# Kernel tuning notes

Measured on AMD Instinct MI355X. Metric: run time of the kernel, lower is better.

The kernel has to match this reference:

```python
import jax, jax.numpy as jnp
import numpy as np
from jax import lax

RF = 19       # receptive field: layers*(kernel-1)+1 = 3*6+1
WINDOW = 12
N_MIX = 2
K = 20        # subgraph_size (top-k per row)
GDEP = 2
ALPHA = 0.05  # propalpha
EPS = 1e-5


def conv2d(x, w, b):
    # x: [N,C,H,W], w: [O,I,1,k], valid conv along time (last) axis
    o = lax.conv_general_dilated(x, w, (1, 1), 'VALID',
                                 dimension_numbers=('NCHW', 'OIHW', 'NCHW'))
    return o + b[None, :, None, None]


def dilated_inception(x, ws, b):
    # ws: kernels [co, ci, k] for k in (2,3,6,7); dilation factor is 1 here
    outs = [lax.conv_general_dilated(x, w[:, :, None, :], (1, 1), 'VALID',
                                     dimension_numbers=('NCHW', 'OIHW', 'NCHW'))
            for w in ws]
    L = outs[-1].shape[-1]  # truncate to shortest (largest kernel) length
    out = jnp.concatenate([o[..., -L:] for o in outs], axis=1)
    return out + b[None, :, None, None]


def build_adj(e1, e2, l1w, l1b, l2w, l2b):
    # e1,e2: [M2,N,D] embedding tables (idx = arange -> full table)
    # torch Linear: y = x @ W.T + b, W: [out,in]
    nv1 = jnp.einsum('mnd,mod->mno', e1, l1w) + l1b[:, None, :]
    nv2 = jnp.einsum('mnd,mod->mno', e2, l2w) + l2b[:, None, :]
    a = jnp.einsum('mnd,mkd->mnk', nv1, nv2)  # [M2, N, N] per-block adjacency
    rows = [jnp.concatenate([a[i * N_MIX + j] for j in range(N_MIX)], axis=1)
            for i in range(N_MIX)]
    adj = jnp.concatenate(rows, axis=0)  # [NT, NT]
    _, t = lax.top_k(adj, K)  # per-row top-k indices
    mask = jnp.zeros_like(adj).at[jnp.arange(adj.shape[0])[:, None], t].set(1.0)
    return adj * mask


def mixprop(x, adj, w, b):
    a = adj + jnp.eye(adj.shape[0], dtype=adj.dtype)
    a = a / jnp.sum(a, axis=1, keepdims=True)  # row-normalize
    h = x
    outs = [h]
    for _ in range(GDEP):
        h = ALPHA * x + (1.0 - ALPHA) * jnp.einsum('ncwl,vw->ncvl', h, a)
        outs.append(h)
    ho = jnp.concatenate(outs, axis=1)  # [B,(GDEP+1)*C,V,L]
    return jnp.einsum('ncvl,oc->novl', ho, w) + b[None, :, None, None]


def layernorm(x, w, b):
    # torch F.layer_norm over all dims except batch; idx = arange -> full affine
    mu = jnp.mean(x, axis=(1, 2, 3), keepdims=True)
    var = jnp.mean((x - mu) ** 2, axis=(1, 2, 3), keepdims=True)
    return (x - mu) * lax.rsqrt(var + EPS) * w[None] + b[None]


def setup_inputs() -> dict:
    keys = iter(jax.random.split(jax.random.key(0), 80))
    def rn(shape, s=0.1):
        return s * jax.random.normal(next(keys), shape, dtype=jnp.float32)
    d = {}
    d['x_in'] = jax.random.normal(next(keys), (32, 12, 500, 4), dtype=jnp.float32)
    d['start_w'] = rn((32, 1, 1, 1)); d['start_b'] = rn((32,))
    d['skip0_w'] = rn((64, 1, 1, 19)); d['skip0_b'] = rn((64,))
    d['emb1'] = rn((3, 4, 500, 40)); d['emb2'] = rn((3, 4, 500, 40))
    d['lin1_w'] = rn((3, 4, 40, 40)); d['lin1_b'] = rn((3, 4, 40))
    d['lin2_w'] = rn((3, 4, 40, 40)); d['lin2_b'] = rn((3, 4, 40))
    d['g1_w'] = rn((3, 32, 96)); d['g1_b'] = rn((3, 32))
    d['g2_w'] = rn((3, 32, 96)); d['g2_b'] = rn((3, 32))
    for pref in ('filt', 'gate'):
        for k in (2, 3, 6, 7):
            d[f'{pref}_w{k}'] = rn((3, 8, 32, k))
        d[f'{pref}_b'] = rn((3, 32))
    for i, L in zip((1, 2, 3), (13, 7, 1)):
        d[f'skip_w{i}'] = rn((64, 32, 1, L)); d[f'skip_b{i}'] = rn((64,))
        d[f'norm_w{i}'] = jnp.ones((32, 1000, L), jnp.float32)
        d[f'norm_b{i}'] = jnp.zeros((32, 1000, L), jnp.float32)
    d['skipE_w'] = rn((64, 32, 1, 1)); d['skipE_b'] = rn((64,))
    d['end1_w'] = rn((128, 64, 1, 1)); d['end1_b'] = rn((128,))
    d['end2_w'] = rn((12, 128, 1, 1)); d['end2_b'] = rn((12,))
    return d


def reference(x_in, start_w, start_b, skip0_w, skip0_b, emb1, emb2,
              lin1_w, lin1_b, lin2_w, lin2_b, g1_w, g1_b, g2_w, g2_b,
              filt_w2, filt_w3, filt_w6, filt_w7, filt_b,
              gate_w2, gate_w3, gate_w6, gate_w7, gate_b,
              skip_w1, skip_b1, skip_w2, skip_b2, skip_w3, skip_b3,
              norm_w1, norm_b1, norm_w2, norm_b2, norm_w3, norm_b3,
              skipE_w, skipE_b, end1_w, end1_b, end2_w, end2_b):
    feat = x_in[..., :-2]  # drop last 2 'time' features
    # split per-mode feature and stack along node dim: [B,T,2N,1]
    inp = jnp.concatenate([feat[..., 0:1], feat[..., 1:2]], axis=2)
    inp = jnp.transpose(inp, (0, 3, 2, 1))  # [B,1,2N,T]
    inp = jnp.pad(inp, ((0, 0), (0, 0), (0, 0), (RF - WINDOW, 0)))
    x = conv2d(inp, start_w, start_b)       # [B,32,1000,19]
    skip = conv2d(inp, skip0_w, skip0_b)    # [B,64,1000,1] (dropout=eval no-op)
    filt_ws = (filt_w2, filt_w3, filt_w6, filt_w7)
    gate_ws = (gate_w2, gate_w3, gate_w6, gate_w7)
    skips = ((skip_w1, skip_b1), (skip_w2, skip_b2), (skip_w3, skip_b3))
    norms = ((norm_w1, norm_b1), (norm_w2, norm_b2), (norm_w3, norm_b3))
    for i in range(3):
        adp = build_adj(emb1[i], emb2[i], lin1_w[i], lin1_b[i], lin2_w[i], lin2_b[i])
        residual = x
        x = mixprop(x, adp, g1_w[i], g1_b[i]) + mixprop(x, adp.T, g2_w[i], g2_b[i])
        f = jnp.tanh(dilated_inception(x, [w[i] for w in filt_ws], filt_b[i]))
        g = jax.nn.sigmoid(dilated_inception(x, [w[i] for w in gate_ws], gate_b[i]))
        x = f * g
        sw, sb = skips[i]
        skip = conv2d(x, sw, sb) + skip
        x = x + residual[..., -x.shape[3]:]
        nw, nb = norms[i]
        x = layernorm(x, nw, nb)
    skip = conv2d(x, skipE_w, skipE_b) + skip
    x = jax.nn.relu(skip)
    x = jax.nn.relu(conv2d(x, end1_w, end1_b))
    return conv2d(x, end2_w, end2_b)  # [B, horizon*out_dim0=12, 1000, 1]
```

## Files before the change

### kernel.cpp

```cpp
#include <hip/hip_runtime.h>
#include <math.h>


#define ALPHA_C 0.05f
#define EPS_C 1e-5f
#define NBC 32
#define CSCT_CAP 140000

__device__ float g_inp[32 * 19 * 1000];
__device__ float g_skip[32 * 64 * 1000];
__device__ __align__(16) float g_nv1[240000];
__device__ __align__(16) float g_nv2[240000];
__device__ __align__(16) int   g_tkcol[60000];
__device__ __align__(16) float g_tkval[60000];
__device__ float g_inv1[3000];
__device__ int   g_colcnt[3000];
__device__ float g_colsum[3000];
__device__ int   g_rp2[3 * 1001 + 1];
__device__ int   g_fill[3000];
__device__ int   g_cscr[60000];
__device__ float g_cscv[60000];
__device__ float g_inv2[3000];
__device__ float g_stats[3 * 64];
__device__ __align__(16) int2 g_pk1T[60000];
__device__ __align__(16) int2 g_cscT[3 * CSCT_CAP];
__device__ int   g_perm[3 * 1024];
__device__ int   g_degT[3 * 1024];
__device__ int   g_iperm[3 * 1000];
__device__ int   g_tOff[3 * 17];
__device__ float g_B0[(size_t)NBC * 32 * 19 * 1000];
__device__ float g_B1[(size_t)NBC * 32 * 19 * 1000];
__device__ float g_B2[(size_t)NBC * 32 * 19 * 1000];
__device__ float g_B3[(size_t)NBC * 32 * 19 * 1000];
__device__ float g_B4[(size_t)NBC * 32 * 19 * 1000];
__device__ float g_B5[(size_t)NBC * 32 * 19 * 1000];

__device__ __forceinline__ float* bufsel(int s)
{
    switch (s) {
        case 0: return g_B0;
        case 1: return g_B1;
        case 2: return g_B2;
        case 3: return g_B3;
        case 4: return g_B4;
        default: return g_B5;
    }
}

__global__ void k_init()
{
    int i = blockIdx.x * 256 + threadIdx.x;
    if (i < 3000) { g_colcnt[i] = 0; g_colsum[i] = 0.f; g_fill[i] = 0; }
    if (i < 192) g_stats[i] = 0.f;
}

__global__ void k_out_zero(float* __restrict__ out, int n)
{
    int i = blockIdx.x * 256 + threadIdx.x;
    if (i < n) out[i] = 0.0f;
}

__global__ void k_marker(float* __restrict__ out, float v)
{
    if (threadIdx.x == 0) out[0] = v;
}


__global__ void k_build_inp(const float* __restrict__ xin)
{
    int i = blockIdx.x * 256 + threadIdx.x;
    if (i >= 32 * 19 * 1000) return;
    int v = i % 1000;
    int t = (i / 1000) % 19;
    int b = i / 19000;
    float val = 0.f;
    if (t >= 7) {
        int tt = t - 7;
        int n = (v < 500) ? v : v - 500;
        int f = (v < 500) ? 0 : 1;
        val = xin[((b * 12 + tt) * 500 + n) * 4 + f];
    }
    g_inp[i] = val;
}

__global__ void k_nv(const float* __restrict__ e1, const float* __restrict__ e2,
                     const float* __restrict__ w1, const float* __restrict__ b1,
                     const float* __restrict__ w2, const float* __restrict__ b2)
{
    int i = blockIdx.x * 256 + threadIdx.x;
    if (i >= 12 * 500 * 40) return;
    int o = i % 40;
    int n = (i / 40) % 500;
    int m = i / (40 * 500);
    const float4* p1 = (const float4*)(e1 + (m * 500 + n) * 40);
    const float4* pw1 = (const float4*)(w1 + (m * 40 + o) * 40);
    const float4* p2 = (const float4*)(e2 + (m * 500 + n) * 40);
    const float4* pw2 = (const float4*)(w2 + (m * 40 + o) * 40);
    float a1 = b1[m * 40 + o], a2 = b2[m * 40 + o];
    for (int d = 0; d < 10; ++d) {
        float4 x1 = p1[d], y1 = pw1[d];
        float4 x2 = p2[d], y2 = pw2[d];
        a1 += x1.x * y1.x; a1 += x1.y * y1.y; a1 += x1.z * y1.z; a1 += x1.w * y1.w;
        a2 += x2.x * y2.x; a2 += x2.y * y2.y; a2 += x2.z * y2.z; a2 += x2.w * y2.w;
    }
    g_nv1[i] = a1;
    g_nv2[i] = a2;
}

__global__ __launch_bounds__(256) void k_adj_topk()
{
    __shared__ float row[1000];
    __shared__ float wvv[4];
    __shared__ int wvi[4];
    __shared__ int selc[20];
    __shared__ float selv[20];
    int li = blockIdx.x / 1000;
    int r = blockIdx.x % 1000;
    int tid = threadIdx.x;
    int wv = tid >> 6, lane = tid & 63;
    int bi = r / 500, n = r % 500;
    for (int c = tid; c < 1000; c += 256) {
        int bj = c / 500, k = c % 500;
        int mg = li * 4 + 2 * bi + bj;
        const float4* a = (const float4*)(g_nv1 + (mg * 500 + n) * 40);
        const float4* b = (const float4*)(g_nv2 + (mg * 500 + k) * 40);
        float acc = 0.f;
#pragma unroll
        for (int d = 0; d < 10; ++d) {
            float4 av = a[d], bv = b[d];
            acc += av.x * bv.x; acc += av.y * bv.y;
            acc += av.z * bv.z; acc += av.w * bv.w;
        }
        row[c] = acc;
    }
    __syncthreads();
    for (int sel = 0; sel < 20; ++sel) {
        float bv = -INFINITY;
        int bidx = 0;
        for (int c = tid; c < 1000; c += 256) {
            float x = row[c];
            if (x > bv) { bv = x; bidx = c; }
        }
#pragma unroll
        for (int m = 1; m < 64; m <<= 1) {
            float ov = __shfl_xor(bv, m);
            int oi = __shfl_xor(bidx, m);
            if (ov > bv || (ov == bv && oi < bidx)) { bv = ov; bidx = oi; }
        }
        if (lane == 0) { wvv[wv] = bv; wvi[wv] = bidx; }
        __syncthreads();
        if (tid == 0) {
            float fv = wvv[0];
            int fi = wvi[0];
#pragma unroll
            for (int k = 1; k < 4; ++k) {
                float ov = wvv[k];
                int oi = wvi[k];
                if (ov > fv || (ov == fv && oi < fi)) { fv = ov; fi = oi; }
            }
            int ci = fi;
            if (ci < 0 || ci > 999) ci = sel;
            selc[sel] = ci;
            selv[sel] = fv;
            g_tkcol[(li * 1000 + r) * 20 + sel] = ci;
            g_tkval[(li * 1000 + r) * 20 + sel] = fv;
            row[ci] = -INFINITY;
        }
        __syncthreads();
    }
    if (tid < 20) {
        atomicAdd(&g_colcnt[li * 1000 + selc[tid]], 1);
        atomicAdd(&g_colsum[li * 1000 + selc[tid]], selv[tid]);
    }
    if (tid == 0) {
        float s = 0.f;
        for (int j = 0; j < 20; ++j) s += selv[j];
        g_inv1[li * 1000 + r] = 1.f / (s + 1.f);
    }
}

__global__ __launch_bounds__(256) void k_scan()
{
    __shared__ int s[1000];
    int li = blockIdx.x;
    int tid = threadIdx.x;
    for (int i = tid; i < 1000; i += 256) s[i] = g_colcnt[li * 1000 + i];
    __syncthreads();
    if (tid == 0) {
        int run = 0;
        for (int i = 0; i < 1000; ++i) { int c = s[i]; s[i] = run; run += c; }
        g_rp2[li * 1001 + 1000] = run;
    }
    __syncthreads();
    for (int i = tid; i < 1000; i += 256) {
        g_rp2[li * 1001 + i] = s[i];
        g_inv2[li * 1000 + i] = 1.f / (g_colsum[li * 1000 + i] + 1.f);
    }
}

__global__ __launch_bounds__(256) void k_permsort()
{
    __shared__ int deg[1000];
    __shared__ int tmax[16];
    int li = blockIdx.x;
    int tid = threadIdx.x;
    for (int v = tid; v < 1000; v += 256)
        deg[v] = g_rp2[li * 1001 + v + 1] - g_rp2[li * 1001 + v];
    __syncthreads();
    for (int v = tid; v < 1000; v += 256) {
        int d = deg[v];
        int r = 0;
        for (int u = 0; u < 1000; ++u) {
            int du = deg[u];
            r += (du > d) || (du == d && u < v);
        }
        g_perm[li * 1024 + r] = v;
        g_degT[li * 1024 + r] = d;
        g_iperm[li * 1000 + v] = r;
        if ((r & 63) == 0) tmax[r >> 6] = d;
    }
    if (tid < 24) {
        g_perm[li * 1024 + 1000 + tid] = -1;
        g_degT[li * 1024 + 1000 + tid] = 0;
    }
    __syncthreads();
    if (tid == 0) {
        int off = 0;
        for (int t = 0; t < 16; ++t) {
            g_tOff[li * 17 + t] = off;
            off += 64 * tmax[t];
        }
        g_tOff[li * 17 + 16] = off;
    }
}

__global__ void k_scatter()
{
    int i = blockIdx.x * 256 + threadIdx.x;
    if (i >= 3 * 20000) return;
    int li = i / 20000;
    int e = i % 20000;
    int r = e / 20;
    int c = g_tkcol[i];
    if (c < 0) c = 0;
    if (c > 999) c = 999;
    float v = g_tkval[i];
    int pos = g_rp2[li * 1001 + c] + atomicAdd(&g_fill[li * 1000 + c], 1);
    if (pos < 0) pos = 0;
    if (pos > 19999) pos = 19999;
    g_cscr[li * 20000 + pos] = r;
    g_cscv[li * 20000 + pos] = v;
}

__global__ void k_packT1()
{
    int i = blockIdx.x * 256 + threadIdx.x;
    if (i >= 60000) return;
    int li = i / 20000;
    int e = i % 20000;
    int v = e / 20, j = e % 20;
    int c1 = g_tkcol[i];
    if (c1 < 0) c1 = 0;
    if (c1 > 999) c1 = 999;
    g_pk1T[li * 20000 + j * 1000 + v] = make_int2(c1 * 16, __float_as_int(g_tkval[i]));
}

__global__ void k_packT2()
{
    int i = blockIdx.x * 256 + threadIdx.x;
    if (i >= 3000) return;
    int li = i / 1000, v = i % 1000;
    int r = g_iperm[li * 1000 + v];
    int t = r >> 6, ln = r & 63;
    int j0 = g_rp2[li * 1001 + v];
    int d = g_rp2[li * 1001 + v + 1] - j0;
    int base = g_tOff[li * 17 + t];
    for (int j = 0; j < d; ++j) {
        int row = g_cscr[li * 20000 + j0 + j];
        if (row < 0) row = 0;
        if (row > 999) row = 999;
        int pos = base + j * 64 + ln;
        if (pos >= 0 && pos < CSCT_CAP)
            g_cscT[li * CSCT_CAP + pos] =
                make_int2(row * 16, __float_as_int(g_cscv[li * 20000 + j0 + j]));
    }
}


__global__ __launch_bounds__(256) void k_skip0(const float* __restrict__ w,
                                               const float* __restrict__ bb)
{
    __shared__ float s_inp[19 * 32];
    __shared__ float s_w[64 * 19];
    int b = blockIdx.y;
    int v0 = blockIdx.x * 32;
    int tid = threadIdx.x;
    for (int i = tid; i < 64 * 19; i += 256) s_w[i] = w[i];
    for (int i = tid; i < 19 * 32; i += 256) {
        int t = i / 32, vl = i % 32;
        int v = v0 + vl;
        s_inp[i] = (v < 1000) ? g_inp[(b * 19 + t) * 1000 + v] : 0.f;
    }
    __syncthreads();
    for (int e = tid; e < 64 * 32; e += 256) {
        int o = e / 32, vl = e % 32;
        int v = v0 + vl;
        if (v >= 1000) continue;
        float acc = bb[o];
#pragma unroll
        for (int t = 0; t < 19; ++t) acc += s_w[o * 19 + t] * s_inp[t * 32 + vl];
        g_skip[(b * 64 + o) * 1000 + v] = acc;
    }
}

__global__ __launch_bounds__(256, 5) void k_prop4(int xsel, int o1s, int o2s, int o3s, int o4s,
                                                  int li, int CH, int li0,
                                                  const float* __restrict__ sw,
                                                  const float* __restrict__ sb)
{
    __shared__ float4 S[2000];
    const float* X = bufsel(xsel);
    float* o1 = bufsel(o1s);
    float* o2 = bufsel(o2s);
    float* o3 = bufsel(o3s);
    float* o4 = bufsel(o4s);
    const int2* pkT = g_pk1T + li * 20000;
    const int2* cT = g_cscT + (size_t)li * CSCT_CAP;
    const int* prm = g_perm + li * 1024;
    const int* dgT = g_degT + li * 1024;
    const int* tOf = g_tOff + li * 17;
    const float* iv1 = g_inv1 + li * 1000;
    const float* iv2 = g_inv2 + li * 1000;
    int n = blockIdx.y;
    int ch0 = blockIdx.x * 4;
    size_t gb = ((size_t)n * CH + ch0) * 1000;
    int tid = threadIdx.x;
    int wv = tid >> 6, lane = tid & 63;
    char* Ub = (char*)S;
    char* Wb = (char*)(S + 1000);
    float4* U4 = S;
    float4* W4 = S + 1000;

    auto csr_hop = [&](const char* sbuf, float4* dst) {
        for (int it = 0; it < 4; ++it) {
            int v = it * 256 + tid;
            if (v >= 1000) break;
            const int2* mp = pkT + v;
            float4 a = *(const float4*)(sbuf + (size_t)v * 16);
#pragma unroll
            for (int jb = 0; jb < 5; ++jb) {
                int2 e0 = mp[(jb * 4 + 0) * 1000];
                int2 e1 = mp[(jb * 4 + 1) * 1000];
                int2 e2 = mp[(jb * 4 + 2) * 1000];
                int2 e3 = mp[(jb * 4 + 3) * 1000];
                float w0 = __int_as_float(e0.y), w1 = __int_as_float(e1.y);
                float w2 = __int_as_float(e2.y), w3 = __int_as_float(e3.y);
                float4 x0 = *(const float4*)(sbuf + e0.x);
                float4 x1 = *(const float4*)(sbuf + e1.x);
                float4 x2 = *(const float4*)(sbuf + e2.x);
                float4 x3 = *(const float4*)(sbuf + e3.x);
                a.x += w0 * x0.x + w1 * x1.x + w2 * x2.x + w3 * x3.x;
                a.y += w0 * x0.y + w1 * x1.y + w2 * x2.y + w3 * x3.y;
                a.z += w0 * x0.z + w1 * x1.z + w2 * x2.z + w3 * x3.z;
                a.w += w0 * x0.w + w1 * x1.w + w2 * x2.w + w3 * x3.w;
            }
            float s = iv1[v];
            a.x *= s; a.y *= s; a.z *= s; a.w *= s;
            dst[v] = a;
        }
    };

    auto csc_hop = [&](const char* sbuf, float4* dst) {
        for (int o = 0; o < 4; ++o) {
            int tile = o * 4 + ((o & 1) ? (3 - wv) : wv);
            int r = tile * 64 + lane;
            int v = prm[r];
            if (v < 0) continue;
            int d = dgT[r];
            const int2* mp = cT + tOf[tile] + lane;
            float4 a = *(const float4*)(sbuf + (size_t)v * 16);
            int j = 0;
            for (; j + 4 <= d; j += 4) {
                int2 e0 = mp[(j + 0) * 64];
                int2 e1 = mp[(j + 1) * 64];
                int2 e2 = mp[(j + 2) * 64];
                int2 e3 = mp[(j + 3) * 64];
                float w0 = __int_as_float(e0.y), w1 = __int_as_float(e1.y);
                float w2 = __int_as_float(e2.y), w3 = __int_as_float(e3.y);
                float4 x0 = *(const float4*)(sbuf + e0.x);
                float4 x1 = *(const float4*)(sbuf + e1.x);
                float4 x2 = *(const float4*)(sbuf + e2.x);
                float4 x3 = *(const float4*)(sbuf + e3.x);
                a.x += w0 * x0.x + w1 * x1.x + w2 * x2.x + w3 * x3.x;
                a.y += w0 * x0.y + w1 * x1.y + w2 * x2.y + w3 * x3.y;
                a.z += w0 * x0.z + w1 * x1.z + w2 * x2.z + w3 * x3.z;
                a.w += w0 * x0.w + w1 * x1.w + w2 * x2.w + w3 * x3.w;
            }
            for (; j < d; ++j) {
                int2 e = mp[j * 64];
                float w = __int_as_float(e.y);
                float4 x = *(const float4*)(sbuf + e.x);
                a.x += w * x.x; a.y += w * x.y; a.z += w * x.z; a.w += w * x.w;
            }
            float s = iv2[v];
            a.x *= s; a.y *= s; a.z *= s; a.w *= s;
            dst[v] = a;
        }
    };

    auto stage_x = [&](float4* dst) {
        if (li0) {
            float swv0 = sw[(ch0 + 0) / 19], sbv0 = sb[(ch0 + 0) / 19];
            float swv1 = sw[(ch0 + 1) / 19], sbv1 = sb[(ch0 + 1) / 19];
            float swv2 = sw[(ch0 + 2) / 19], sbv2 = sb[(ch0 + 2) / 19];
            float swv3 = sw[(ch0 + 3) / 19], sbv3 = sb[(ch0 + 3) / 19];
            const float* i0 = g_inp + (n * 19 + (ch0 + 0) % 19) * 1000;
            const float* i1 = g_inp + (n * 19 + (ch0 + 1) % 19) * 1000;
            const float* i2 = g_inp + (n * 19 + (ch0 + 2) % 19) * 1000;
            const float* i3 = g_inp + (n * 19 + (ch0 + 3) % 19) * 1000;
            for (int it = 0; it < 4; ++it) {
                int v = it * 256 + tid;
                if (v >= 1000) break;
                float4 t;
                t.x = swv0 * i0[v] + sbv0;
                t.y = swv1 * i1[v] + sbv1;
                t.z = swv2 * i2[v] + sbv2;
                t.w = swv3 * i3[v] + sbv3;
                dst[v] = t;
            }
        } else {
            for (int it = 0; it < 4; ++it) {
                int v = it * 256 + tid;
                if (v >= 1000) break;
                float4 t;
                t.x = X[gb + v];
                t.y = X[gb + 1000 + v];
                t.z = X[gb + 2000 + v];
                t.w = X[gb + 3000 + v];
                dst[v] = t;
            }
        }
    };

    stage_x(U4);
    __syncthreads();

    csr_hop(Ub, W4);
    __syncthreads();

    for (int it = 0; it < 4; ++it) {
        int v = it * 256 + tid;
        if (v >= 1000) break;
        float4 t = W4[v];
        o1[gb + v] = t.x;
        o1[gb + 1000 + v] = t.y;
        o1[gb + 2000 + v] = t.z;
        o1[gb + 3000 + v] = t.w;
    }
    csr_hop(Wb, U4);
    __syncthreads();

    for (int it = 0; it < 4; ++it) {
        int v = it * 256 + tid;
        if (v >= 1000) break;
        float4 t = U4[v];
        o2[gb + v] = t.x;
        o2[gb + 1000 + v] = t.y;
        o2[gb + 2000 + v] = t.z;
        o2[gb + 3000 + v] = t.w;
    }
    stage_x(W4);
    __syncthreads();

    csc_hop(Wb, U4);
    __syncthreads();

    for (int it = 0; it < 4; ++it) {
        int v = it * 256 + tid;
        if (v >= 1000) break;
        float4 t = U4[v];
        o3[gb + v] = t.x;
        o3[gb + 1000 + v] = t.y;
        o3[gb + 2000 + v] = t.z;
        o3[gb + 3000 + v] = t.w;
    }
    csc_hop(Ub, W4);
    __syncthreads();

    for (int it = 0; it < 4; ++it) {
        int v = it * 256 + tid;
        if (v >= 1000) break;
        float4 t = W4[v];
        o4[gb + v] = t.x;
        o4[gb + 1000 + v] = t.y;
        o4[gb + 2000 + v] = t.z;
        o4[gb + 3000 + v] = t.w;
    }
}

__global__ __launch_bounds__(256) void k_mix(int xs, int h1s, int h2s, int h3s, int h4s, int ms,
                                             const float* __restrict__ g1w, const float* __restrict__ g2w,
                                             const float* __restrict__ g1b, const float* __restrict__ g2b,
                                             int P, int li0,
                                             const float* __restrict__ sw_,
                                             const float* __restrict__ sb_)
{
    __shared__ float sW[5 * 1024];
    __shared__ float sB[32];
    __shared__ float sWS[32];
    __shared__ float sSB[32];
    int tid = threadIdx.x;
    const float A = ALPHA_C, Bq = 1.f - ALPHA_C;
    for (int i = tid; i < 1024; i += 256) {
        int o = i >> 5, c = i & 31;
        float w1 = g1w[o * 96 + 32 + c], w2 = g1w[o * 96 + 64 + c];
        float w3 = g2w[o * 96 + 32 + c], w4 = g2w[o * 96 + 64 + c];
        sW[i]        = g1w[o * 96 + c] + g2w[o * 96 + c] + A * (w1 + w2 + w3 + w4);
        sW[1024 + i] = Bq * (w1 + A * w2);
        sW[2048 + i] = Bq * Bq * w2;
        sW[3072 + i] = Bq * (w3 + A * w4);
        sW[4096 + i] = Bq * Bq * w4;
    }
    if (tid < 32) sB[tid] = g1b[tid] + g2b[tid];
    __syncthreads();
    if (li0 && tid < 32) {
        float as = 0.f, ab = 0.f;
        for (int c = 0; c < 32; ++c) {
            float w = sW[tid * 32 + c];
            as += w * sw_[c];
            ab += w * sb_[c];
        }
        sWS[tid] = as;
        sSB[tid] = ab;
    }
    if (li0) __syncthreads();
    int n = blockIdx.y;
    int p = blockIdx.x * 256 + tid;
    if (p >= P) return;
    const float* srcs[5] = {bufsel(xs), bufsel(h1s), bufsel(h2s), bufsel(h3s), bufsel(h4s)};
    float acc[32];
    int st0;
    if (li0) {
        float xv = g_inp[(size_t)n * 19000 + p];
#pragma unroll
        for (int o = 0; o < 32; ++o) acc[o] = sB[o] + sSB[o] + sWS[o] * xv;
        st0 = 1;
    } else {
#pragma unroll
        for (int o = 0; o < 32; ++o) acc[o] = sB[o];
        st0 = 0;
    }
    for (int st = st0; st < 5; ++st) {
        const float* src = srcs[st] + (size_t)n * 32 * P + p;
        const float* w = &sW[st * 1024];
        for (int c = 0; c < 32; ++c) {
            float hv = src[(size_t)c * P];
#pragma unroll
            for (int o = 0; o < 32; ++o) acc[o] += w[o * 32 + c] * hv;
        }
    }
    float* XM = bufsel(ms) + (size_t)n * 32 * P + p;
#pragma unroll
    for (int o = 0; o < 32; ++o) XM[(size_t)o * P] = acc[o];
}

template <int LIN>
__global__ __launch_bounds__(256) void k_incept(int xmsel, int xgsel,
                                                const float* __restrict__ fw2, const float* __restrict__ fw3,
                                                const float* __restrict__ fw6, const float* __restrict__ fw7,
                                                const float* __restrict__ fb,
                                                const float* __restrict__ gw2, const float* __restrict__ gw3,
                                                const float* __restrict__ gw6, const float* __restrict__ gw7,
                                                const float* __restrict__ gb,
                                                const float* __restrict__ skw, const float* __restrict__ skb)
{
    const int LOUT = LIN - 6;
    const float* XM = bufsel(xmsel);
    float* XG = bufsel(xgsel);
    __shared__ float sx[32 * 8 * LIN];
    __shared__ float sxg[32 * 8 * LOUT];
    int tid = threadIdx.x;
    int n = blockIdx.y, v0 = blockIdx.x * 8;
    for (int i = tid; i < 32 * LIN * 8; i += 256) {
        int vl = i & 7;
        int l = (i >> 3) % LIN;
        int c = i / (8 * LIN);
        sx[(c * 8 + vl) * LIN + l] = XM[(((size_t)n * 32 + c) * LIN + l) * 1000 + v0 + vl];
    }
    __syncthreads();
    int co = tid >> 3, vl = tid & 7;
    int s = co >> 3, co_s = co & 7;
    const int ksz[4] = {2, 3, 6, 7};
    int k = ksz[s];
    const float* fw = (s == 0) ? fw2 : ((s == 1) ? fw3 : ((s == 2) ? fw6 : fw7));
    const float* gw = (s == 0) ? gw2 : ((s == 1) ? gw3 : ((s == 2) ? gw6 : gw7));
    float accf[LOUT], accg[LOUT];
    float bf = fb[co], bg = gb[co];
#pragma unroll
    for (int l = 0; l < LOUT; ++l) { accf[l] = bf; accg[l] = bg; }
    for (int c = 0; c < 32; ++c) {
        const float* xp = &sx[(c * 8 + vl) * LIN];
        for (int j = 0; j < k; ++j) {
            float wf = fw[(co_s * 32 + c) * k + j];
            float wg = gw[(co_s * 32 + c) * k + j];
            int base = 7 - k + j;
#pragma unroll
            for (int l = 0; l < LOUT; ++l) {
                float xv = xp[base + l];
                accf[l] += wf * xv;
                accg[l] += wg * xv;
            }
        }
    }
    size_t ob = ((size_t)n * 32 + co) * LOUT * 1000 + v0 + vl;
#pragma unroll
    for (int l = 0; l < LOUT; ++l) {
        float g = tanhf(accf[l]) * (1.f / (1.f + expf(-accg[l])));
        XG[ob + (size_t)l * 1000] = g;
        sxg[(co * 8 + vl) * LOUT + l] = g;
    }
    __syncthreads();
    int obk = tid >> 3;
    for (int half = 0; half < 2; ++half) {
        int o = obk + 32 * half;
        float acc = skb[o];
        for (int c = 0; c < 32; ++c) {
            const float* wp = &skw[((size_t)o * 32 + c) * LOUT];
            const float* xp = &sxg[(c * 8 + vl) * LOUT];
#pragma unroll
            for (int l = 0; l < LOUT; ++l) acc += wp[l] * xp[l];
        }
        size_t si = ((size_t)n * 64 + o) * 1000 + v0 + vl;
        g_skip[si] += acc;
    }
}

__global__ __launch_bounds__(256) void k_resid_stats(int xnsel, int xpsel,
                                                     int li, int LIN, int LOUT, int li0,
                                                     const float* __restrict__ sw_,
                                                     const float* __restrict__ sb_)
{
    float* XN = bufsel(xnsel);
    const float* Xp = bufsel(xpsel);
    float* stats = g_stats + li * 64;
    int n = blockIdx.y;
    int S = 32 * LOUT * 1000;
    int tid = threadIdx.x;
    int gsz = gridDim.x * 256;
    float sum = 0.f, ss = 0.f;
    for (int idx = blockIdx.x * 256 + tid; idx < S; idx += gsz) {
        int v = idx % 1000;
        int l = (idx / 1000) % LOUT;
        int c = idx / (1000 * LOUT);
        float r;
        if (li0)
            r = sw_[c] * g_inp[(n * 19 + l + 6) * 1000 + v] + sb_[c];
        else
            r = Xp[(((size_t)n * 32 + c) * LIN + l + (LIN - LOUT)) * 1000 + v];
        float y = XN[(size_t)n * S + idx] + r;
        XN[(size_t)n * S + idx] = y;
        sum += y;
        ss += y * y;
    }
    __shared__ float s1[256], s2[256];
    s1[tid] = sum;
    s2[tid] = ss;
    __syncthreads();
    for (int s = 128; s > 0; s >>= 1) {
        if (tid < s) { s1[tid] += s1[tid + s]; s2[tid] += s2[tid + s]; }
        __syncthreads();
    }
    if (tid == 0) {
        atomicAdd(&stats[n * 2], s1[0]);
        atomicAdd(&stats[n * 2 + 1], s2[0]);
    }
}

__global__ void k_norm(int xnsel, const float* __restrict__ nw,
                       const float* __restrict__ nb, int li, int LOUT)
{
    float* XN = bufsel(xnsel);
    const float* stats = g_stats + li * 64;
    int S = 32 * LOUT * 1000;
    long long total = (long long)NBC * S;
    long long stride = (long long)gridDim.x * 256;
    for (long long i = (long long)blockIdx.x * 256 + threadIdx.x; i < total; i += stride) {
        int n = (int)(i / S);
        int rem = (int)(i % S);
        int v = rem % 1000;
        int l = (rem / 1000) % LOUT;
        int c = rem / (1000 * LOUT);
        int widx = (c * 1000 + v) * LOUT + l;
        float cnt = (float)S;
        float mu = stats[n * 2] / cnt;
        float var = stats[n * 2 + 1] / cnt - mu * mu;
        float rs = rsqrtf(var + EPS_C);
        XN[i] = (XN[i] - mu) * rs * nw[widx] + nb[widx];
    }
}

__global__ __launch_bounds__(256) void k_final(int xsel,
                                               const float* __restrict__ ew, const float* __restrict__ eb,
                                               const float* __restrict__ e1w, const float* __restrict__ e1b,
                                               const float* __restrict__ e2w, const float* __restrict__ e2b,
                                               float* __restrict__ out)
{
    const float* X = bufsel(xsel);
    __shared__ float sxf[32 * 16];
    __shared__ float sk[64 * 16];
    __shared__ float s1[64 * 16];
    __shared__ float s2[128 * 16];
    int b = blockIdx.y, v0 = blockIdx.x * 16;
    int tid = threadIdx.x;
    for (int i = tid; i < 512; i += 256) {
        int c = i / 16, vl = i & 15;
        int v = v0 + vl;
        sxf[i] = (v < 1000) ? X[((size_t)b * 32 + c) * 1000 + v] : 0.f;
    }
    for (int i = tid; i < 1024; i += 256) {
        int o = i / 16, vl = i & 15;
        int v = v0 + vl;
        sk[i] = (v < 1000) ? g_skip[((size_t)b * 64 + o) * 1000 + v] : 0.f;
    }
    __syncthreads();
    for (int i = tid; i < 1024; i += 256) {
        int o = i / 16, vl = i & 15;
        float acc = sk[i] + eb[o];
        for (int c = 0; c < 32; ++c) acc += ew[o * 32 + c] * sxf[c * 16 + vl];
        s1[i] = fmaxf(acc, 0.f);
    }
    __syncthreads();
    for (int i = tid; i < 2048; i += 256) {
        int o = i / 16, vl = i & 15;
        float acc = e1b[o];
        for (int c = 0; c < 64; ++c) acc += e1w[o * 64 + c] * s1[c * 16 + vl];
        s2[i] = fmaxf(acc, 0.f);
    }
    __syncthreads();
    if (tid < 192) {
        int o = tid / 16, vl = tid & 15;
        int v = v0 + vl;
        if (v < 1000) {
            float acc = e2b[o];
            for (int c = 0; c < 128; ++c) acc += e2w[o * 128 + c] * s2[c * 16 + vl];
            out[((size_t)b * 12 + o) * 1000 + v] = acc;
        }
    }
}


static const int SZ_SORT[43] = {240000,240000,128,8192,12,1536,96,1536,2304,4608,
                                5376,96,9216,96,9216,96,1536,2304,4608,5376,
                                480,19200,480,19200,416000,224000,32000,416000,224000,32000,
                                64,1216,64,2048,64,64,64,26624,14336,2048,32,32,768000};
static const int SZ_DICT[43] = {768000,32,32,1216,64,240000,240000,19200,480,19200,
                                480,9216,96,9216,96,1536,2304,4608,5376,96,
                                1536,2304,4608,5376,96,26624,64,416000,416000,14336,
                                64,224000,224000,2048,64,32000,32000,2048,64,8192,128,1536,12};
static const int SZ_SIG[43]  = {768000,32,32,1216,64,240000,240000,19200,480,19200,
                                480,9216,96,9216,96,1536,2304,4608,5376,96,
                                1536,2304,4608,5376,96,26624,64,14336,64,2048,
                                64,416000,416000,224000,224000,32000,32000,2048,64,8192,128,1536,12};

extern "C" void kernel_launch(void* const* d_in, const int* in_sizes, int n_in,
                              void* d_out, int out_size, void* d_ws, size_t ws_size,
                              hipStream_t stream)
{
    (void)d_ws; (void)ws_size;
    const float *x_in, *start_w, *start_b, *skip0_w, *skip0_b;
    const float *emb1, *emb2, *lin1_w, *lin1_b, *lin2_w, *lin2_b;
    const float *g1_w, *g1_b, *g2_w, *g2_b;
    const float *filt_w[4], *filt_b, *gate_w[4], *gate_b;
    const float *skw[3], *skb[3], *nww[3], *nbb[3];
    const float *skipE_w, *skipE_b, *end1_w, *end1_b, *end2_w, *end2_b;
    float* outp = (float*)d_out;
    auto P = [&](int i) { return (const float*)d_in[i]; };
    auto match = [&](const int* tab) {
        if (n_in < 43) return false;
        for (int i = 0; i < 43; ++i) if (in_sizes[i] != tab[i]) return false;
        return true;
    };

    int fam = -1;
    if (match(SZ_SORT)) fam = 0;
    else if (match(SZ_DICT)) fam = 1;
    else if (match(SZ_SIG)) fam = 2;

    if (fam == 0) {
        emb1 = P(0); emb2 = P(1); end1_b = P(2); end1_w = P(3); end2_b = P(4); end2_w = P(5);
        filt_b = P(6); filt_w[0] = P(7); filt_w[1] = P(8); filt_w[2] = P(9); filt_w[3] = P(10);
        g1_b = P(11); g1_w = P(12); g2_b = P(13); g2_w = P(14);
        gate_b = P(15); gate_w[0] = P(16); gate_w[1] = P(17); gate_w[2] = P(18); gate_w[3] = P(19);
        lin1_b = P(20); lin1_w = P(21); lin2_b = P(22); lin2_w = P(23);
        nbb[0] = P(24); nbb[1] = P(25); nbb[2] = P(26);
        nww[0] = P(27); nww[1] = P(28); nww[2] = P(29);
        skip0_b = P(30); skip0_w = P(31); skipE_b = P(32); skipE_w = P(33);
        skb[0] = P(34); skb[1] = P(35); skb[2] = P(36);
        skw[0] = P(37); skw[1] = P(38); skw[2] = P(39);
        start_b = P(40); start_w = P(41); x_in = P(42);
    } else if (fam == 1 || fam == 2) {
        x_in = P(0); start_w = P(1); start_b = P(2); skip0_w = P(3); skip0_b = P(4);
        emb1 = P(5); emb2 = P(6); lin1_w = P(7); lin1_b = P(8); lin2_w = P(9); lin2_b = P(10);
        g1_w = P(11); g1_b = P(12); g2_w = P(13); g2_b = P(14);
        filt_w[0] = P(15); filt_w[1] = P(16); filt_w[2] = P(17); filt_w[3] = P(18); filt_b = P(19);
        gate_w[0] = P(20); gate_w[1] = P(21); gate_w[2] = P(22); gate_w[3] = P(23); gate_b = P(24);
        if (fam == 1) {
            skw[0] = P(25); skb[0] = P(26); nww[0] = P(27); nbb[0] = P(28);
            skw[1] = P(29); skb[1] = P(30); nww[1] = P(31); nbb[1] = P(32);
            skw[2] = P(33); skb[2] = P(34); nww[2] = P(35); nbb[2] = P(36);
        } else {
            skw[0] = P(25); skb[0] = P(26); skw[1] = P(27); skb[1] = P(28);
            skw[2] = P(29); skb[2] = P(30);
            nww[0] = P(31); nbb[0] = P(32); nww[1] = P(33); nbb[1] = P(34);
            nww[2] = P(35); nbb[2] = P(36);
        }
        skipE_w = P(37); skipE_b = P(38); end1_w = P(39); end1_b = P(40);
        end2_w = P(41); end2_b = P(42);
    } else {
        k_out_zero<<<(out_size + 255) / 256, 256, 0, stream>>>(outp, out_size);
        k_marker<<<1, 64, 0, stream>>>(outp, 8192.0f);
        return;
    }

    k_init<<<12, 256, 0, stream>>>();
    k_build_inp<<<(32 * 19 * 1000 + 255) / 256, 256, 0, stream>>>(x_in);
    k_nv<<<(240000 + 255) / 256, 256, 0, stream>>>(emb1, emb2, lin1_w, lin1_b, lin2_w, lin2_b);
    k_adj_topk<<<3000, 256, 0, stream>>>();
    k_scan<<<3, 256, 0, stream>>>();
    k_permsort<<<3, 256, 0, stream>>>();
    k_scatter<<<(60000 + 255) / 256, 256, 0, stream>>>();
    k_packT1<<<(60000 + 255) / 256, 256, 0, stream>>>();
    k_packT2<<<12, 256, 0, stream>>>();

    k_skip0<<<dim3(32, NBC), 256, 0, stream>>>(skip0_w, skip0_b);

    int X = 0;
    int LIN = 19;
    for (int li = 0; li < 3; ++li) {
        int LOUT = LIN - 6;
        int Pp = 1000 * LIN;
        int li0 = (li == 0) ? 1 : 0;
        int hb[4], hn = 0;
        for (int b = 0; b < 6 && hn < 4; ++b)
            if (b != X && b != 1) hb[hn++] = b;
        int h1 = hb[0], h2 = hb[1], h3 = hb[2], h4 = hb[3];
        int CH = 32 * LIN;
        dim3 gg((unsigned)(CH / 4), NBC);

        k_prop4<<<gg, 256, 0, stream>>>(X, h1, h2, h3, h4, li, CH, li0, start_w, start_b);

        k_mix<<<dim3((Pp + 255) / 256, NBC), 256, 0, stream>>>(X, h1, h2, h3, h4, 1,
            g1_w + li * 3072, g2_w + li * 3072, g1_b + li * 32, g2_b + li * 32, Pp,
            li0, start_w, start_b);

        int XG = h1;
        if (LIN == 19)
            k_incept<19><<<dim3(125, NBC), 256, 0, stream>>>(1, XG,
                filt_w[0] + li * 512, filt_w[1] + li * 768, filt_w[2] + li * 1536, filt_w[3] + li * 1792,
                filt_b + li * 32,
                gate_w[0] + li * 512, gate_w[1] + li * 768, gate_w[2] + li * 1536, gate_w[3] + li * 1792,
                gate_b + li * 32, skw[li], skb[li]);
        else if (LIN == 13)
            k_incept<13><<<dim3(125, NBC), 256, 0, stream>>>(1, XG,
                filt_w[0] + li * 512, filt_w[1] + li * 768, filt_w[2] + li * 1536, filt_w[3] + li * 1792,
                filt_b + li * 32,
                gate_w[0] + li * 512, gate_w[1] + li * 768, gate_w[2] + li * 1536, gate_w[3] + li * 1792,
                gate_b + li * 32, skw[li], skb[li]);
        else
            k_incept<7><<<dim3(125, NBC), 256, 0, stream>>>(1, XG,
                filt_w[0] + li * 512, filt_w[1] + li * 768, filt_w[2] + li * 1536, filt_w[3] + li * 1792,
                filt_b + li * 32,
                gate_w[0] + li * 512, gate_w[1] + li * 768, gate_w[2] + li * 1536, gate_w[3] + li * 1792,
                gate_b + li * 32, skw[li], skb[li]);

        k_resid_stats<<<dim3(16, NBC), 256, 0, stream>>>(XG, X, li, LIN, LOUT,
                                                         li0, start_w, start_b);
        k_norm<<<2048, 256, 0, stream>>>(XG, nww[li], nbb[li], li, LOUT);

        X = XG;
        LIN = LOUT;
    }
    k_final<<<dim3(63, NBC), 256, 0, stream>>>(X, skipE_w, skipE_b,
                                               end1_w, end1_b, end2_w, end2_b, outp);
}
```

Baseline: 2.671 ms.

## Fuse residual add and norm stats into inception kernel; reuse staged input in prop

The residual add and the per-sample layernorm sum and sum-of-squares are folded into the inception epilogue, with a wave-shuffle reduction and atomics. This removes the separate k_resid_stats launch and its extra read and write of the activation tensor. In k_prop4 the staged input is kept in shared memory across the CSR and CSC hops, so it is no longer reloaded. The CSR hops also write their outputs to global memory directly instead of through a separate copy loop. The inception kernel takes on more per-thread work and extra global loads for the residual, and atomics now come from every block.

```diff
diff --git a/kernel.cpp b/kernel.cpp
--- a/kernel.cpp
+++ b/kernel.cpp
@@ -341,7 +341,7 @@
     float4* U4 = S;
     float4* W4 = S + 1000;
 
-    auto csr_hop = [&](const char* sbuf, float4* dst) {
+    auto csr_hop = [&](const char* sbuf, float4* dst, float* gout) {
         for (int it = 0; it < 4; ++it) {
             int v = it * 256 + tid;
             if (v >= 1000) break;
@@ -366,7 +366,11 @@
             }
             float s = iv1[v];
             a.x *= s; a.y *= s; a.z *= s; a.w *= s;
-            dst[v] = a;
+            if (dst) dst[v] = a;
+            gout[gb + v] = a.x;
+            gout[gb + 1000 + v] = a.y;
+            gout[gb + 2000 + v] = a.z;
+            gout[gb + 3000 + v] = a.w;
         }
     };
 
@@ -408,89 +412,64 @@
         }
     };
 
-    auto stage_x = [&](float4* dst) {
-        if (li0) {
-            float swv0 = sw[(ch0 + 0) / 19], sbv0 = sb[(ch0 + 0) / 19];
-            float swv1 = sw[(ch0 + 1) / 19], sbv1 = sb[(ch0 + 1) / 19];
-            float swv2 = sw[(ch0 + 2) / 19], sbv2 = sb[(ch0 + 2) / 19];
-            float swv3 = sw[(ch0 + 3) / 19], sbv3 = sb[(ch0 + 3) / 19];
-            const float* i0 = g_inp + (n * 19 + (ch0 + 0) % 19) * 1000;
-            const float* i1 = g_inp + (n * 19 + (ch0 + 1) % 19) * 1000;
-            const float* i2 = g_inp + (n * 19 + (ch0 + 2) % 19) * 1000;
-            const float* i3 = g_inp + (n * 19 + (ch0 + 3) % 19) * 1000;
-            for (int it = 0; it < 4; ++it) {
-                int v = it * 256 + tid;
-                if (v >= 1000) break;
-                float4 t;
-                t.x = swv0 * i0[v] + sbv0;
-                t.y = swv1 * i1[v] + sbv1;
-                t.z = swv2 * i2[v] + sbv2;
-                t.w = swv3 * i3[v] + sbv3;
-                dst[v] = t;
-            }
-        } else {
-            for (int it = 0; it < 4; ++it) {
-                int v = it * 256 + tid;
-                if (v >= 1000) break;
-                float4 t;
-                t.x = X[gb + v];
-                t.y = X[gb + 1000 + v];
-                t.z = X[gb + 2000 + v];
-                t.w = X[gb + 3000 + v];
-                dst[v] = t;
-            }
-        }
-    };
-
-    stage_x(U4);
-    __syncthreads();
-
-    csr_hop(Ub, W4);
+    if (li0) {
+        float swv0 = sw[(ch0 + 0) / 19], sbv0 = sb[(ch0 + 0) / 19];
+        float swv1 = sw[(ch0 + 1) / 19], sbv1 = sb[(ch0 + 1) / 19];
+        float swv2 = sw[(ch0 + 2) / 19], sbv2 = sb[(ch0 + 2) / 19];
+        float swv3 = sw[(ch0 + 3) / 19], sbv3 = sb[(ch0 + 3) / 19];
+        const float* i0 = g_inp + (n * 19 + (ch0 + 0) % 19) * 1000;
+        const float* i1 = g_inp + (n * 19 + (ch0 + 1) % 19) * 1000;
+        const float* i2 = g_inp + (n * 19 + (ch0 + 2) % 19) * 1000;
+        const float* i3 = g_inp + (n * 19 + (ch0 + 3) % 19) * 1000;
+        for (int it = 0; it < 4; ++it) {
+            int v = it * 256 + tid;
+            if (v >= 1000) break;
+            float4 t;
+            t.x = swv0 * i0[v] + sbv0;
+            t.y = swv1 * i1[v] + sbv1;
+            t.z = swv2 * i2[v] + sbv2;
+            t.w = swv3 * i3[v] + sbv3;
+            U4[v] = t;
+        }
+    } else {
+        for (int it = 0; it < 4; ++it) {
+            int v = it * 256 + tid;
+            if (v >= 1000) break;
+            float4 t;
+            t.x = X[gb + v];
+            t.y = X[gb + 1000 + v];
+            t.z = X[gb + 2000 + v];
+            t.w = X[gb + 3000 + v];
+            U4[v] = t;
+        }
+    }
+    __syncthreads();
+
+    csr_hop(Ub, W4, o1);
+    __syncthreads();
+
+    csr_hop(Wb, (float4*)nullptr, o2);
+    __syncthreads();
+
+    csc_hop(Ub, W4);
     __syncthreads();
 
     for (int it = 0; it < 4; ++it) {
         int v = it * 256 + tid;
         if (v >= 1000) break;
         float4 t = W4[v];
-        o1[gb + v] = t.x;
-        o1[gb + 1000 + v] = t.y;
-        o1[gb + 2000 + v] = t.z;
-        o1[gb + 3000 + v] = t.w;
-    }
-    csr_hop(Wb, U4);
+        o3[gb + v] = t.x;
+        o3[gb + 1000 + v] = t.y;
+        o3[gb + 2000 + v] = t.z;
+        o3[gb + 3000 + v] = t.w;
+    }
+    csc_hop(Wb, U4);
     __syncthreads();
 
     for (int it = 0; it < 4; ++it) {
         int v = it * 256 + tid;
         if (v >= 1000) break;
         float4 t = U4[v];
-        o2[gb + v] = t.x;
-        o2[gb + 1000 + v] = t.y;
-        o2[gb + 2000 + v] = t.z;
-        o2[gb + 3000 + v] = t.w;
-    }
-    stage_x(W4);
-    __syncthreads();
-
-    csc_hop(Wb, U4);
-    __syncthreads();
-
-    for (int it = 0; it < 4; ++it) {
-        int v = it * 256 + tid;
-        if (v >= 1000) break;
-        float4 t = U4[v];
-        o3[gb + v] = t.x;
-        o3[gb + 1000 + v] = t.y;
-        o3[gb + 2000 + v] = t.z;
-        o3[gb + 3000 + v] = t.w;
-    }
-    csc_hop(Ub, W4);
-    __syncthreads();
-
-    for (int it = 0; it < 4; ++it) {
-        int v = it * 256 + tid;
-        if (v >= 1000) break;
-        float4 t = W4[v];
         o4[gb + v] = t.x;
         o4[gb + 1000 + v] = t.y;
         o4[gb + 2000 + v] = t.z;
@@ -565,20 +544,26 @@
 }
 
 template <int LIN>
-__global__ __launch_bounds__(256) void k_incept(int xmsel, int xgsel,
+__global__ __launch_bounds__(256) void k_incept(int xmsel, int xgsel, int xpsel,
                                                 const float* __restrict__ fw2, const float* __restrict__ fw3,
                                                 const float* __restrict__ fw6, const float* __restrict__ fw7,
                                                 const float* __restrict__ fb,
                                                 const float* __restrict__ gw2, const float* __restrict__ gw3,
                                                 const float* __restrict__ gw6, const float* __restrict__ gw7,
                                                 const float* __restrict__ gb,
-                                                const float* __restrict__ skw, const float* __restrict__ skb)
+                                                const float* __restrict__ skw, const float* __restrict__ skb,
+                                                int li, int li0,
+                                                const float* __restrict__ sw_,
+                                                const float* __restrict__ sb_)
 {
     const int LOUT = LIN - 6;
     const float* XM = bufsel(xmsel);
     float* XG = bufsel(xgsel);
+    const float* Xp = bufsel(xpsel);
+    float* stats = g_stats + li * 64;
     __shared__ float sx[32 * 8 * LIN];
     __shared__ float sxg[32 * 8 * LOUT];
+    __shared__ float ws1[4], ws2[4];
     int tid = threadIdx.x;
     int n = blockIdx.y, v0 = blockIdx.x * 8;
     for (int i = tid; i < 32 * LIN * 8; i += 256) {
@@ -613,11 +598,22 @@
         }
     }
     size_t ob = ((size_t)n * 32 + co) * LOUT * 1000 + v0 + vl;
+    float lsum = 0.f, lss = 0.f;
+    float swc = li0 ? sw_[co] : 0.f;
+    float sbc = li0 ? sb_[co] : 0.f;
 #pragma unroll
     for (int l = 0; l < LOUT; ++l) {
         float g = tanhf(accf[l]) * (1.f / (1.f + expf(-accg[l])));
-        XG[ob + (size_t)l * 1000] = g;
+        float r;
+        if (li0)
+            r = swc * g_inp[(n * 19 + l + 6) * 1000 + v0 + vl] + sbc;
+        else
+            r = Xp[(((size_t)n * 32 + co) * LIN + l + 6) * 1000 + v0 + vl];
+        float y = g + r;
+        XG[ob + (size_t)l * 1000] = y;
         sxg[(co * 8 + vl) * LOUT + l] = g;
+        lsum += y;
+        lss += y * y;
     }
     __syncthreads();
     int obk = tid >> 3;
@@ -633,46 +629,19 @@
         size_t si = ((size_t)n * 64 + o) * 1000 + v0 + vl;
         g_skip[si] += acc;
     }
-}
-
-__global__ __launch_bounds__(256) void k_resid_stats(int xnsel, int xpsel,
-                                                     int li, int LIN, int LOUT, int li0,
-                                                     const float* __restrict__ sw_,
-                                                     const float* __restrict__ sb_)
-{
-    float* XN = bufsel(xnsel);
-    const float* Xp = bufsel(xpsel);
-    float* stats = g_stats + li * 64;
-    int n = blockIdx.y;
-    int S = 32 * LOUT * 1000;
-    int tid = threadIdx.x;
-    int gsz = gridDim.x * 256;
-    float sum = 0.f, ss = 0.f;
-    for (int idx = blockIdx.x * 256 + tid; idx < S; idx += gsz) {
-        int v = idx % 1000;
-        int l = (idx / 1000) % LOUT;
-        int c = idx / (1000 * LOUT);
-        float r;
-        if (li0)
-            r = sw_[c] * g_inp[(n * 19 + l + 6) * 1000 + v] + sb_[c];
-        else
-            r = Xp[(((size_t)n * 32 + c) * LIN + l + (LIN - LOUT)) * 1000 + v];
-        float y = XN[(size_t)n * S + idx] + r;
-        XN[(size_t)n * S + idx] = y;
-        sum += y;
-        ss += y * y;
-    }
-    __shared__ float s1[256], s2[256];
-    s1[tid] = sum;
-    s2[tid] = ss;
-    __syncthreads();
-    for (int s = 128; s > 0; s >>= 1) {
-        if (tid < s) { s1[tid] += s1[tid + s]; s2[tid] += s2[tid + s]; }
-        __syncthreads();
-    }
+#pragma unroll
+    for (int m = 1; m < 64; m <<= 1) {
+        lsum += __shfl_xor(lsum, m);
+        lss += __shfl_xor(lss, m);
+    }
+    int wvi = tid >> 6;
+    if ((tid & 63) == 0) { ws1[wvi] = lsum; ws2[wvi] = lss; }
+    __syncthreads();
     if (tid == 0) {
-        atomicAdd(&stats[n * 2], s1[0]);
-        atomicAdd(&stats[n * 2 + 1], s2[0]);
+        float t1 = ws1[0] + ws1[1] + ws1[2] + ws1[3];
+        float t2 = ws2[0] + ws2[1] + ws2[2] + ws2[3];
+        atomicAdd(&stats[n * 2], t1);
+        atomicAdd(&stats[n * 2 + 1], t2);
     }
 }
 
@@ -855,26 +824,24 @@
 
         int XG = h1;
         if (LIN == 19)
-            k_incept<19><<<dim3(125, NBC), 256, 0, stream>>>(1, XG,
+            k_incept<19><<<dim3(125, NBC), 256, 0, stream>>>(1, XG, X,
                 filt_w[0] + li * 512, filt_w[1] + li * 768, filt_w[2] + li * 1536, filt_w[3] + li * 1792,
                 filt_b + li * 32,
                 gate_w[0] + li * 512, gate_w[1] + li * 768, gate_w[2] + li * 1536, gate_w[3] + li * 1792,
-                gate_b + li * 32, skw[li], skb[li]);
+                gate_b + li * 32, skw[li], skb[li], li, li0, start_w, start_b);
         else if (LIN == 13)
-            k_incept<13><<<dim3(125, NBC), 256, 0, stream>>>(1, XG,
+            k_incept<13><<<dim3(125, NBC), 256, 0, stream>>>(1, XG, X,
                 filt_w[0] + li * 512, filt_w[1] + li * 768, filt_w[2] + li * 1536, filt_w[3] + li * 1792,
                 filt_b + li * 32,
                 gate_w[0] + li * 512, gate_w[1] + li * 768, gate_w[2] + li * 1536, gate_w[3] + li * 1792,
-                gate_b + li * 32, skw[li], skb[li]);
+                gate_b + li * 32, skw[li], skb[li], li, li0, start_w, start_b);
         else
-            k_incept<7><<<dim3(125, NBC), 256, 0, stream>>>(1, XG,
+            k_incept<7><<<dim3(125, NBC), 256, 0, stream>>>(1, XG, X,
                 filt_w[0] + li * 512, filt_w[1] + li * 768, filt_w[2] + li * 1536, filt_w[3] + li * 1792,
                 filt_b + li * 32,
                 gate_w[0] + li * 512, gate_w[1] + li * 768, gate_w[2] + li * 1536, gate_w[3] + li * 1792,
-                gate_b + li * 32, skw[li], skb[li]);
-
-        k_resid_stats<<<dim3(16, NBC), 256, 0, stream>>>(XG, X, li, LIN, LOUT,
-                                                         li0, start_w, start_b);
+                gate_b + li * 32, skw[li], skb[li], li, li0, start_w, start_b);
+
         k_norm<<<2048, 256, 0, stream>>>(XG, nww[li], nbb[li], li, LOUT);
 
         X = XG;
```

Measured after the change: 2.618 ms. -2.0%, faster.
